# Performance work log

Measured on AMD Instinct MI355X. Metric: run time of the kernel, lower is better.

The kernel has to match this reference:

```python
import jax, jax.numpy as jnp
import numpy as np
import math

D_MODEL = 1024
NUM_HEADS = 16
HEAD_DIM = D_MODEL // NUM_HEADS


def setup_inputs() -> dict:
    key = jax.random.key(0)
    k1, k2, k3, k4 = jax.random.split(key, 4)
    x = jax.random.normal(k1, (1, 4096, D_MODEL), dtype=jnp.float32)
    # torch nn.Linear weights: [out_features, in_features]
    s = 1.0 / math.sqrt(D_MODEL)
    w_qkv = jax.random.uniform(k2, (3 * D_MODEL, D_MODEL), jnp.float32, -s, s)
    w_out = jax.random.uniform(k3, (D_MODEL, D_MODEL), jnp.float32, -s, s)
    b_out = jax.random.uniform(k4, (D_MODEL,), jnp.float32, -s, s)
    return {"x": x, "w_qkv": w_qkv, "w_out": w_out, "b_out": b_out}


def reference(x, w_qkv, w_out, b_out):
    B, T, C = x.shape
    qkv = (x @ w_qkv.T).reshape(B, T, 3, NUM_HEADS, HEAD_DIM)
    q, k, v = qkv[:, :, 0], qkv[:, :, 1], qkv[:, :, 2]  # [B,T,H,Dh]
    scores = jnp.einsum('bthd,bshd->bhts', q, k) / jnp.sqrt(jnp.float32(HEAD_DIM))
    weights = jax.nn.softmax(scores, axis=-1)  # [B,H,T,S]
    attn = jnp.einsum('bhts,bshd->bthd', weights, v).reshape(B, T, C)
    return attn @ w_out.T + b_out
```

## Files before the change

### kernel.cpp

```cpp
#include <hip/hip_runtime.h>
#include <hip/hip_bf16.h>
#include <math.h>

#define T_SEQ 4096
#define NH 16
#define HD 64
#define C_DIM 1024
#define N_QKV 3072

typedef __bf16 bf16x8 __attribute__((ext_vector_type(8)));
typedef __bf16 bf16x2 __attribute__((ext_vector_type(2)));
typedef float f32x4 __attribute__((ext_vector_type(4)));
typedef float f32x16 __attribute__((ext_vector_type(16)));
typedef unsigned short u16x8 __attribute__((ext_vector_type(8)));
typedef unsigned short u16x4 __attribute__((ext_vector_type(4)));
typedef unsigned int u32x4 __attribute__((ext_vector_type(4)));

__device__ __forceinline__ unsigned short f2bf(float f) {
  unsigned u = __builtin_bit_cast(unsigned, f);
  u += 0x7FFFu + ((u >> 16) & 1u);
  return (unsigned short)(u >> 16);
}

__device__ __forceinline__ bf16x8 lds_frag(const unsigned short* p) {
  return __builtin_bit_cast(bf16x8, *reinterpret_cast<const u16x8*>(p));
}

__device__ __forceinline__ void gload_lds16(const unsigned short* g, unsigned short* l) {
  __builtin_amdgcn_global_load_lds(
      (const __attribute__((address_space(1))) unsigned int*)(uintptr_t)(const void*)g,
      (__attribute__((address_space(3))) unsigned int*)(uintptr_t)(void*)l, 16, 0, 0);
}

__global__ void convert_kernel(const float* __restrict__ x,
                               const float* __restrict__ wqkv,
                               const float* __restrict__ wout,
                               unsigned short* __restrict__ xb,
                               unsigned short* __restrict__ wqkvb,
                               unsigned short* __restrict__ woutb) {
  const int NX = T_SEQ * C_DIM;
  const int NW = N_QKV * C_DIM;
  const int NO = C_DIM * C_DIM;
  int idx = blockIdx.x * blockDim.x + threadIdx.x;
  int i = idx * 4;
  if (i >= NX + NW + NO) return;
  const float* src;
  unsigned short* dst;
  if (i < NX)            { src = x + i;                dst = xb + i; }
  else if (i < NX + NW)  { src = wqkv + (i - NX);      dst = wqkvb + (i - NX); }
  else                   { src = wout + (i - NX - NW); dst = woutb + (i - NX - NW); }
  float4 v = *reinterpret_cast<const float4*>(src);
  u16x4 o;
  o[0] = f2bf(v.x); o[1] = f2bf(v.y); o[2] = f2bf(v.z); o[3] = f2bf(v.w);
  *reinterpret_cast<u16x4*>(dst) = o;
}

template <bool F32OUT>
__global__ __launch_bounds__(256) void gemm_bt(
    const unsigned short* __restrict__ A, const unsigned short* __restrict__ Bm,
    unsigned short* __restrict__ Cb, float* __restrict__ Cf,
    const float* __restrict__ bias, int M, int N, int K,
    int scale_cols, float ascale) {
  __shared__ __align__(16) unsigned short As[128 * 64];
  __shared__ __align__(16) unsigned short Bs[128 * 64];
  const int tid = threadIdx.x;
  const int lane = tid & 63, wid = tid >> 6;
  const int l15 = lane & 15, g = lane >> 4;
  const int nbn = N >> 7;
  const int bm = blockIdx.x / nbn, bn = blockIdx.x % nbn;
  const int wm = wid >> 1, wn = wid & 1;

  f32x4 acc[4][4];
  const f32x4 zero = {0.f, 0.f, 0.f, 0.f};
#pragma unroll
  for (int m = 0; m < 4; m++)
#pragma unroll
    for (int n = 0; n < 4; n++) acc[m][n] = zero;

  for (int k0 = 0; k0 < K; k0 += 64) {
    __syncthreads();
#pragma unroll
    for (int i = 0; i < 4; i++) {
      int c = tid + i * 256;
      int row = c >> 3, slot = c & 7;
      int col = slot ^ (row & 7);
      gload_lds16(A + (size_t)(bm * 128 + row) * K + k0 + col * 8, &As[c * 8]);
      gload_lds16(Bm + (size_t)(bn * 128 + row) * K + k0 + col * 8, &Bs[c * 8]);
    }
    __syncthreads();
#pragma unroll
    for (int kk = 0; kk < 2; kk++) {
      bf16x8 af[4], bfr[4];
#pragma unroll
      for (int m = 0; m < 4; m++) {
        int row = wm * 64 + m * 16 + l15;
        af[m] = lds_frag(reinterpret_cast<const unsigned short*>(
            reinterpret_cast<const char*>(As) + row * 128 + ((kk * 64 + g * 16) ^ ((l15 & 7) << 4))));
      }
#pragma unroll
      for (int n = 0; n < 4; n++) {
        int row = wn * 64 + n * 16 + l15;
        bfr[n] = lds_frag(reinterpret_cast<const unsigned short*>(
            reinterpret_cast<const char*>(Bs) + row * 128 + ((kk * 64 + g * 16) ^ ((l15 & 7) << 4))));
      }
#pragma unroll
      for (int m = 0; m < 4; m++)
#pragma unroll
        for (int n = 0; n < 4; n++)
          acc[m][n] = __builtin_amdgcn_mfma_f32_16x16x32_bf16(af[m], bfr[n], acc[m][n], 0, 0, 0);
    }
  }
#pragma unroll
  for (int m = 0; m < 4; m++) {
    int row0 = bm * 128 + wm * 64 + m * 16 + g * 4;
#pragma unroll
    for (int n = 0; n < 4; n++) {
      int col = bn * 128 + wn * 64 + n * 16 + l15;
      float bi = 0.f;
      if (F32OUT) bi = bias[col];
      float cs = (col < scale_cols) ? ascale : 1.0f;
#pragma unroll
      for (int r = 0; r < 4; r++) {
        float v = acc[m][n][r];
        if (F32OUT) Cf[(size_t)(row0 + r) * N + col] = v + bi;
        else        Cb[(size_t)(row0 + r) * N + col] = f2bf(v * cs);
      }
    }
  }
}

__global__ __launch_bounds__(256, 2) void attn_kernel(
    const unsigned short* __restrict__ qkv,
    unsigned short* __restrict__ attn) {
  __shared__ __align__(16) unsigned short smem[2 * 2 * 4864];
  const int tid = threadIdx.x;
  const int lane = tid & 63, wid = tid >> 6;
  const int qw = wid & 1, str = wid >> 1;
  const int stid = qw * 64 + lane;
  const int l31 = lane & 31, hi = lane >> 5;
  const int sw = (blockIdx.x & 7) * 64 + (blockIdx.x >> 3);
  const int h = sw >> 5;
  const int qb = sw & 31;
  const int t0 = qb * 128 + qw * 64;
  const int q = l31;
  const int kvbase = str * (T_SEQ / 2);
  const int NT = (T_SEQ / 2) / 32;

  unsigned short* Sbase = &smem[str * 2 * 4864];

  const int krow = stid >> 2, ks = stid & 3;
  const int kp = stid & 15, vd0 = (stid >> 4) * 8;

  bf16x8 qf[2][4];
#pragma unroll
  for (int j = 0; j < 2; j++)
#pragma unroll
    for (int ds = 0; ds < 4; ds++) {
      const unsigned short* p =
          qkv + (size_t)(t0 + j * 32 + q) * N_QKV + h * HD + ds * 16 + hi * 8;
      qf[j][ds] = __builtin_bit_cast(bf16x8, *reinterpret_cast<const u16x8*>(p));
    }

  float l_run[2] = {0.f, 0.f};
  f32x16 o[2][2];
  const f32x16 zero16 = {0.f};
  o[0][0] = zero16; o[0][1] = zero16; o[1][0] = zero16; o[1][1] = zero16;
  f32x16 minit;
#pragma unroll
  for (int i = 0; i < 16; i++) minit[i] = -4.0f;

  u16x8 kreg[2], vreg[2];
  {
    const unsigned short* kb = qkv + (size_t)(kvbase + krow) * N_QKV + C_DIM + h * HD + ks * 16;
    kreg[0] = *reinterpret_cast<const u16x8*>(kb);
    kreg[1] = *reinterpret_cast<const u16x8*>(kb + 8);
    const unsigned short* vb = qkv + (size_t)(kvbase + 2 * kp) * N_QKV + 2 * C_DIM + h * HD + vd0;
    vreg[0] = *reinterpret_cast<const u16x8*>(vb);
    vreg[1] = *reinterpret_cast<const u16x8*>(vb + N_QKV);
  }

  for (int t = 0; t < NT; t++) {
    unsigned short* Kb = Sbase + (t & 1) * 4864;
    unsigned short* Vb = Kb + 2304;
    *reinterpret_cast<u16x8*>(&Kb[krow * 72 + ks * 16]) = kreg[0];
    *reinterpret_cast<u16x8*>(&Kb[krow * 72 + ks * 16 + 8]) = kreg[1];
#pragma unroll
    for (int jj = 0; jj < 8; jj++) {
      unsigned pk = (unsigned)vreg[0][jj] | ((unsigned)vreg[1][jj] << 16);
      *reinterpret_cast<unsigned*>(&Vb[(vd0 + jj) * 40 + 2 * kp]) = pk;
    }
    if (t < NT - 1) {
      const int kv0 = kvbase + (t + 1) * 32;
      const unsigned short* kb = qkv + (size_t)(kv0 + krow) * N_QKV + C_DIM + h * HD + ks * 16;
      kreg[0] = *reinterpret_cast<const u16x8*>(kb);
      kreg[1] = *reinterpret_cast<const u16x8*>(kb + 8);
      const unsigned short* vb = qkv + (size_t)(kv0 + 2 * kp) * N_QKV + 2 * C_DIM + h * HD + vd0;
      vreg[0] = *reinterpret_cast<const u16x8*>(vb);
      vreg[1] = *reinterpret_cast<const u16x8*>(vb + N_QKV);
    }
    __syncthreads();

    f32x16 s[2];
    s[0] = minit; s[1] = minit;
    __builtin_amdgcn_s_setprio(1);
#pragma unroll
    for (int ds = 0; ds < 4; ds++) {
      bf16x8 kf = lds_frag(&Kb[l31 * 72 + ds * 16 + hi * 8]);
      s[0] = __builtin_amdgcn_mfma_f32_32x32x16_bf16(kf, qf[0][ds], s[0], 0, 0, 0);
      s[1] = __builtin_amdgcn_mfma_f32_32x32x16_bf16(kf, qf[1][ds], s[1], 0, 0, 0);
    }
    __builtin_amdgcn_s_setprio(0);

    unsigned wA[2][8];
#pragma unroll
    for (int j = 0; j < 2; j++) {
      float psum[8];
#pragma unroll
      for (int i = 0; i < 8; i++) {
        float pa = __builtin_amdgcn_exp2f(s[j][2 * i]);
        float pb = __builtin_amdgcn_exp2f(s[j][2 * i + 1]);
        bf16x2 pk = {(__bf16)pa, (__bf16)pb};
        wA[j][i] = __builtin_bit_cast(unsigned, pk);
        psum[i] = pa + pb;
      }
#pragma unroll
      for (int i = 0; i < 4; i++) psum[i] += psum[i + 4];
      l_run[j] += (psum[0] + psum[2]) + (psum[1] + psum[3]);
#pragma unroll
      for (int base = 0; base < 8; base += 4)
#pragma unroll
        for (int k = 0; k < 2; k++) {
          unsigned A = wA[j][base + k];
          unsigned B = wA[j][base + k + 2];
          asm("v_permlane32_swap_b32 %0, %1" : "+v"(A), "+v"(B));
          wA[j][base + k]     = A;
          wA[j][base + k + 2] = B;
        }
    }

    u32x4 g00 = {wA[0][0], wA[0][1], wA[0][2], wA[0][3]};
    u32x4 g01 = {wA[0][4], wA[0][5], wA[0][6], wA[0][7]};
    u32x4 g10 = {wA[1][0], wA[1][1], wA[1][2], wA[1][3]};
    u32x4 g11 = {wA[1][4], wA[1][5], wA[1][6], wA[1][7]};
    bf16x8 pf00 = __builtin_bit_cast(bf16x8, g00);
    bf16x8 pf01 = __builtin_bit_cast(bf16x8, g01);
    bf16x8 pf10 = __builtin_bit_cast(bf16x8, g10);
    bf16x8 pf11 = __builtin_bit_cast(bf16x8, g11);
    __builtin_amdgcn_s_setprio(1);
#pragma unroll
    for (int dblk = 0; dblk < 2; dblk++) {
      bf16x8 vf0 = lds_frag(&Vb[(dblk * 32 + l31) * 40 + hi * 8]);
      bf16x8 vf1 = lds_frag(&Vb[(dblk * 32 + l31) * 40 + 16 + hi * 8]);
      o[0][dblk] = __builtin_amdgcn_mfma_f32_32x32x16_bf16(vf0, pf00, o[0][dblk], 0, 0, 0);
      o[0][dblk] = __builtin_amdgcn_mfma_f32_32x32x16_bf16(vf1, pf01, o[0][dblk], 0, 0, 0);
      o[1][dblk] = __builtin_amdgcn_mfma_f32_32x32x16_bf16(vf0, pf10, o[1][dblk], 0, 0, 0);
      o[1][dblk] = __builtin_amdgcn_mfma_f32_32x32x16_bf16(vf1, pf11, o[1][dblk], 0, 0, 0);
    }
    __builtin_amdgcn_s_setprio(0);
  }

  float* ob = reinterpret_cast<float*>(&smem[0]);
  float* lb = ob + 8192;
  const int midx = qw * 64 + lane;
#pragma unroll
  for (int j = 0; j < 2; j++) {
    __syncthreads();
    if (str == 1) {
#pragma unroll
      for (int dblk = 0; dblk < 2; dblk++)
#pragma unroll
        for (int r = 0; r < 16; r++)
          ob[(dblk * 16 + r) * 128 + midx] = o[j][dblk][r];
      lb[midx] = l_run[j];
    }
    __syncthreads();
    if (str == 0) {
#pragma unroll
      for (int dblk = 0; dblk < 2; dblk++)
#pragma unroll
        for (int r = 0; r < 16; r++)
          o[j][dblk][r] += ob[(dblk * 16 + r) * 128 + midx];
      l_run[j] += lb[midx];
    }
  }

  if (str == 0) {
#pragma unroll
    for (int j = 0; j < 2; j++) {
      float lr = l_run[j];
      float inv = 1.f / (lr + __shfl_xor(lr, 32));
      const int t = t0 + j * 32 + q;
#pragma unroll
      for (int dblk = 0; dblk < 2; dblk++)
#pragma unroll
        for (int qd = 0; qd < 4; qd++) {
          u16x4 w;
#pragma unroll
          for (int i = 0; i < 4; i++) w[i] = f2bf(o[j][dblk][qd * 4 + i] * inv);
          *reinterpret_cast<u16x4*>(
              &attn[(size_t)t * C_DIM + h * HD + dblk * 32 + qd * 8 + hi * 4]) = w;
        }
    }
  }
}

extern "C" void kernel_launch(void* const* d_in, const int* in_sizes, int n_in,
                              void* d_out, int out_size, void* d_ws, size_t ws_size,
                              hipStream_t stream) {
  const float* x     = (const float*)d_in[0];
  const float* w_qkv = (const float*)d_in[1];
  const float* w_out = (const float*)d_in[2];
  const float* b_out = (const float*)d_in[3];
  float* out = (float*)d_out;
  char* ws = (char*)d_ws;
  unsigned short* xb    = (unsigned short*)(ws);
  unsigned short* wqkvb = (unsigned short*)(ws + (8u << 20));
  unsigned short* woutb = (unsigned short*)(ws + (14u << 20));
  unsigned short* qkvb  = (unsigned short*)(ws + (16u << 20));
  unsigned short* attnb = (unsigned short*)(ws + (40u << 20));

  const float QSCALE = 0.125f * 1.44269504f;

  convert_kernel<<<8192, 256, 0, stream>>>(x, w_qkv, w_out, xb, wqkvb, woutb);
  gemm_bt<false><<<768, 256, 0, stream>>>(xb, wqkvb, qkvb, nullptr, nullptr,
                                          T_SEQ, N_QKV, C_DIM, C_DIM, QSCALE);
  attn_kernel<<<512, 256, 0, stream>>>(qkvb, attnb);
  gemm_bt<true><<<256, 256, 0, stream>>>(attnb, woutb, nullptr, out, b_out,
                                         T_SEQ, C_DIM, C_DIM, 0, 1.0f);
}
```

Before: 144.4 us.

## Fuse x fp32-to-bf16 conversion into QKV GEMM load and swizzle block order

Drops the separate conversion pass over x: the QKV GEMM now reads fp32 x directly, converts it to bf16 in registers and writes it to LDS, while the weights are still pre-converted. This removes a 16MB read plus 8MB write of x and its bf16 reload. It also remaps block indices in an XCD-style interleave (blockIdx & 7) to improve L2 locality. In exchange, the A-tile load moves from async global_load_lds to synchronous register loads plus conversion, and each x element is reconverted by all 24 N-blocks, which could hurt GEMM latency hiding.

```diff
diff --git a/kernel.cpp b/kernel.cpp
--- a/kernel.cpp
+++ b/kernel.cpp
@@ -32,42 +32,42 @@
       (__attribute__((address_space(3))) unsigned int*)(uintptr_t)(void*)l, 16, 0, 0);
 }
 
-__global__ void convert_kernel(const float* __restrict__ x,
-                               const float* __restrict__ wqkv,
+__global__ void convert_kernel(const float* __restrict__ wqkv,
                                const float* __restrict__ wout,
-                               unsigned short* __restrict__ xb,
                                unsigned short* __restrict__ wqkvb,
                                unsigned short* __restrict__ woutb) {
-  const int NX = T_SEQ * C_DIM;
   const int NW = N_QKV * C_DIM;
   const int NO = C_DIM * C_DIM;
   int idx = blockIdx.x * blockDim.x + threadIdx.x;
   int i = idx * 4;
-  if (i >= NX + NW + NO) return;
+  if (i >= NW + NO) return;
   const float* src;
   unsigned short* dst;
-  if (i < NX)            { src = x + i;                dst = xb + i; }
-  else if (i < NX + NW)  { src = wqkv + (i - NX);      dst = wqkvb + (i - NX); }
-  else                   { src = wout + (i - NX - NW); dst = woutb + (i - NX - NW); }
+  if (i < NW) { src = wqkv + i;        dst = wqkvb + i; }
+  else        { src = wout + (i - NW); dst = woutb + (i - NW); }
   float4 v = *reinterpret_cast<const float4*>(src);
   u16x4 o;
   o[0] = f2bf(v.x); o[1] = f2bf(v.y); o[2] = f2bf(v.z); o[3] = f2bf(v.w);
   *reinterpret_cast<u16x4*>(dst) = o;
 }
 
-template <bool F32OUT>
+template <bool F32OUT, bool AF32>
 __global__ __launch_bounds__(256) void gemm_bt(
-    const unsigned short* __restrict__ A, const unsigned short* __restrict__ Bm,
+    const void* __restrict__ Avoid, const unsigned short* __restrict__ Bm,
     unsigned short* __restrict__ Cb, float* __restrict__ Cf,
     const float* __restrict__ bias, int M, int N, int K,
     int scale_cols, float ascale) {
   __shared__ __align__(16) unsigned short As[128 * 64];
   __shared__ __align__(16) unsigned short Bs[128 * 64];
+  const unsigned short* A16 = (const unsigned short*)Avoid;
+  const float* A32 = (const float*)Avoid;
   const int tid = threadIdx.x;
   const int lane = tid & 63, wid = tid >> 6;
   const int l15 = lane & 15, g = lane >> 4;
   const int nbn = N >> 7;
-  const int bm = blockIdx.x / nbn, bn = blockIdx.x % nbn;
+  const int nwg = gridDim.x;
+  const int swzb = (blockIdx.x & 7) * (nwg >> 3) + (blockIdx.x >> 3);
+  const int bm = swzb / nbn, bn = swzb % nbn;
   const int wm = wid >> 1, wn = wid & 1;
 
   f32x4 acc[4][4];
@@ -84,7 +84,16 @@
       int c = tid + i * 256;
       int row = c >> 3, slot = c & 7;
       int col = slot ^ (row & 7);
-      gload_lds16(A + (size_t)(bm * 128 + row) * K + k0 + col * 8, &As[c * 8]);
+      if (AF32) {
+        const float* ap = A32 + (size_t)(bm * 128 + row) * K + k0 + col * 8;
+        float4 v0 = *reinterpret_cast<const float4*>(ap);
+        float4 v1 = *reinterpret_cast<const float4*>(ap + 4);
+        bf16x8 w = {(__bf16)v0.x, (__bf16)v0.y, (__bf16)v0.z, (__bf16)v0.w,
+                    (__bf16)v1.x, (__bf16)v1.y, (__bf16)v1.z, (__bf16)v1.w};
+        *reinterpret_cast<bf16x8*>(&As[c * 8]) = w;
+      } else {
+        gload_lds16(A16 + (size_t)(bm * 128 + row) * K + k0 + col * 8, &As[c * 8]);
+      }
       gload_lds16(Bm + (size_t)(bn * 128 + row) * K + k0 + col * 8, &Bs[c * 8]);
     }
     __syncthreads();
@@ -313,7 +322,6 @@
   const float* b_out = (const float*)d_in[3];
   float* out = (float*)d_out;
   char* ws = (char*)d_ws;
-  unsigned short* xb    = (unsigned short*)(ws);
   unsigned short* wqkvb = (unsigned short*)(ws + (8u << 20));
   unsigned short* woutb = (unsigned short*)(ws + (14u << 20));
   unsigned short* qkvb  = (unsigned short*)(ws + (16u << 20));
@@ -321,10 +329,10 @@
 
   const float QSCALE = 0.125f * 1.44269504f;
 
-  convert_kernel<<<8192, 256, 0, stream>>>(x, w_qkv, w_out, xb, wqkvb, woutb);
-  gemm_bt<false><<<768, 256, 0, stream>>>(xb, wqkvb, qkvb, nullptr, nullptr,
-                                          T_SEQ, N_QKV, C_DIM, C_DIM, QSCALE);
+  convert_kernel<<<4096, 256, 0, stream>>>(w_qkv, w_out, wqkvb, woutb);
+  gemm_bt<false, true><<<768, 256, 0, stream>>>(x, wqkvb, qkvb, nullptr, nullptr,
+                                                T_SEQ, N_QKV, C_DIM, C_DIM, QSCALE);
   attn_kernel<<<512, 256, 0, stream>>>(qkvb, attnb);
-  gemm_bt<true><<<256, 256, 0, stream>>>(attnb, woutb, nullptr, out, b_out,
-                                         T_SEQ, C_DIM, C_DIM, 0, 1.0f);
-}
+  gemm_bt<true, false><<<256, 256, 0, stream>>>(attnb, woutb, nullptr, out, b_out,
+                                                T_SEQ, C_DIM, C_DIM, 0, 1.0f);
+}
```

Result: slower. 149.1 us (+3.3%).
